# Performance work log

Hardware: AMD Instinct MI355X
Metric: run time of the kernel (lower is better)

## Reference

```python
import jax, jax.numpy as jnp
import numpy as np

IMG = 512
STRIDES = (8, 16, 32, 64, 128)
AREAS = np.array([(IMG // s) ** 2 for s in STRIDES])  # [4096,1024,256,64,16]
A_TOTAL = int(AREAS.sum())  # 5456
LEVELS = 5
TOP_K = 3
MAX_OBJ = 32
NUM_CLASSES = 80
BATCH = 16


def _detections():
    # [LEVELS, A_TOTAL] one-hot level membership per anchor (tf.pad of ones)
    det = np.zeros((LEVELS, A_TOTAL), np.float32)
    off = 0
    for i, a in enumerate(AREAS):
        det[i, off:off + a] = 1.0
        off += a
    return jnp.asarray(det)


def focal_loss(y_true, y_pred, alpha=0.25, gamma=2.0):
    # y_pred are sigmoid probabilities; sum over classes -> [B, A]
    p = jnp.clip(y_pred, 1e-7, 1.0 - 1e-7)
    ce = -(y_true * jnp.log(p) + (1.0 - y_true) * jnp.log(1.0 - p))
    alpha_t = y_true * alpha + (1.0 - y_true) * (1.0 - alpha)
    pt = y_true * (1.0 - p) + (1.0 - y_true) * p
    return jnp.sum(alpha_t * pt ** gamma * ce, axis=-1)


def giou_loss(y_true, y_pred):
    # ltrb distance encoding (all >= 0) -> per-anchor GIoU loss [B, A]
    tl, tt, tr, tb = (y_true[..., i] for i in range(4))
    pl, pt_, pr, pb = (y_pred[..., i] for i in range(4))
    area_t = (tl + tr) * (tt + tb)
    area_p = (pl + pr) * (pt_ + pb)
    inter = (jnp.minimum(tl, pl) + jnp.minimum(tr, pr)) * (jnp.minimum(tt, pt_) + jnp.minimum(tb, pb))
    union = area_t + area_p - inter
    iou = inter / jnp.maximum(union, 1e-7)
    enc = (jnp.maximum(tl, pl) + jnp.maximum(tr, pr)) * (jnp.maximum(tt, pt_) + jnp.maximum(tb, pb))
    giou = iou - (enc - union) / jnp.maximum(enc, 1e-7)
    return 1.0 - giou


def dwlm(total_loss, ind, bbox_cnt):
    # total_loss [B,A], ind [B,A] int, bbox_cnt [B] int
    det = _detections()                                   # [L, A]
    obj_ids = jnp.arange(MAX_OBJ)                         # [O]
    valid = obj_ids[None, :] < bbox_cnt[:, None]          # [B, O]
    obj_mask = (ind[:, None, :] == obj_ids[None, :, None]).astype(total_loss.dtype)  # [B,O,A]
    det_mask = obj_mask[:, :, None, :] * det[None, None]  # [B,O,L,A]
    obj_l_sum = jnp.einsum('ba,bola->bol', total_loss, det_mask)
    cnt = jnp.sum(det_mask, axis=-1)                      # [B,O,L]
    mean = obj_l_sum / jnp.maximum(1.0, cnt)
    lmax = jnp.max(mean, axis=-1, keepdims=True) + 1e-5
    mean = jnp.where(mean == 0.0, lmax, mean)
    lmin = jnp.min(mean, axis=-1, keepdims=True)
    target = 1.0 - (mean - lmin) / (lmax - lmin)          # [B,O,L]
    kth = jax.lax.top_k(target, TOP_K)[0][..., -1:]
    target = jnp.where(target >= kth, target, 0.0)
    target = jnp.where(valid[..., None], target, 0.0)     # drop padded objects
    return jnp.einsum('bol,bola->ba', target, det_mask)   # scatter-sum back to anchors


def setup_inputs() -> dict:
    key = jax.random.key(0)
    k = jax.random.split(key, 6)
    return {
        'cls_pred': jax.random.uniform(k[0], (BATCH, A_TOTAL, NUM_CLASSES), jnp.float32),
        'loc_pred': jax.random.uniform(k[1], (BATCH, A_TOTAL, 4), jnp.float32),
        'cls_tar': jax.random.uniform(k[2], (BATCH, A_TOTAL, NUM_CLASSES + 2), jnp.float32),
        'loc_tar': jax.random.uniform(k[3], (BATCH, A_TOTAL, 4), jnp.float32),
        'ind_tar': jax.random.randint(k[4], (BATCH, A_TOTAL, 1), 0, MAX_OBJ, jnp.int32),
        'bboxes_cnt': jax.random.randint(k[5], (BATCH, 1), 0, MAX_OBJ, jnp.int32),
    }


def reference(cls_pred, loc_pred, cls_tar, loc_tar, ind_tar, bboxes_cnt):
    cls_loss = focal_loss(cls_tar[..., :-2], cls_pred)
    loc_loss = giou_loss(loc_tar, loc_pred)
    dwlm_out = dwlm(cls_loss + loc_loss, ind_tar[..., 0], bboxes_cnt[..., 0])
    pos_mask = cls_tar[..., -1]
    dwlm_out_masked = jnp.where(pos_mask > 0.0, dwlm_out, 1.0)
    return dwlm_out_masked[..., None], pos_mask
```

## Files before the change

kernel.cpp:

```cpp
#include <hip/hip_runtime.h>

constexpr int A_TOTAL = 5456;
constexpr int BATCH = 16;
constexpr int NUM_CLASSES = 80;
constexpr int NUM_CH = NUM_CLASSES + 2;
constexpr int MAX_OBJ = 32;
constexpr int LEVELS = 5;
constexpr int BINS = MAX_OBJ * LEVELS;
constexpr int BLK_L = 1024;
constexpr int NSLOT = 16;
constexpr int APB = A_TOTAL / NSLOT;
constexpr int PASS = BLK_L / 4;
constexpr int BLK_G = 256;
constexpr int NBLK_G = (A_TOTAL + BLK_G - 1) / BLK_G;

__device__ __forceinline__ int lev_of(int a) {
    return (a < 4096) ? 0 : (a < 5120) ? 1 : (a < 5376) ? 2 : (a < 5440) ? 3 : 4;
}

__global__ void __launch_bounds__(BLK_L)
loss_accum_kernel(const float* __restrict__ cls_pred,
                  const float* __restrict__ loc_pred,
                  const float* __restrict__ cls_tar,
                  const float* __restrict__ loc_tar,
                  const int*   __restrict__ ind_tar,
                  float* __restrict__ p_sum,
                  float* __restrict__ p_cnt,
                  float* __restrict__ out) {
    __shared__ float s_sum[BINS];
    __shared__ float s_cnt[BINS];
    const int t = threadIdx.x;
    if (t < BINS) { s_sum[t] = 0.f; s_cnt[t] = 0.f; }
    __syncthreads();

    const int b = blockIdx.y;
    const int j = blockIdx.x;
    const int q = t & 3;
    const int r = t >> 2;

    #pragma unroll
    for (int base = 0; base < APB; base += PASS) {
        const int al = base + r;
        const bool valid = al < APB;

        float4 p4[5];
        float2 ta[5], tb[5];
        float4 T, P;
        float  pos = 0.f;
        size_t row = 0;
        int a = 0;

        if (valid) {
            a = j * APB + al;
            row = (size_t)b * A_TOTAL + a;
            const float4* pred4 = (const float4*)cls_pred + row * 20 + q;
            const float2* tar2  = (const float2*)cls_tar  + row * 41 + 2 * q;
            #pragma unroll
            for (int jj = 0; jj < 5; ++jj) {
                p4[jj] = pred4[4 * jj];
                ta[jj] = tar2[8 * jj];
                tb[jj] = tar2[8 * jj + 1];
            }
            T   = ((const float4*)(loc_tar  + row * 4))[0];
            P   = ((const float4*)(loc_pred + row * 4))[0];
            pos = cls_tar[row * NUM_CH + (NUM_CH - 1)];
        }

        float fl = 0.f;
        if (valid) {
            #pragma unroll
            for (int jj = 0; jj < 5; ++jj) {
                float ps[4] = {p4[jj].x, p4[jj].y, p4[jj].z, p4[jj].w};
                float ts[4] = {ta[jj].x, ta[jj].y, tb[jj].x, tb[jj].y};
                #pragma unroll
                for (int k = 0; k < 4; ++k) {
                    float p  = fminf(fmaxf(ps[k], 1e-7f), 1.0f - 1e-7f);
                    float tt = ts[k];
                    float ce = -(tt * __logf(p) + (1.f - tt) * __logf(1.f - p));
                    float alpha_t = tt * 0.25f + (1.f - tt) * 0.75f;
                    float pt = tt * (1.f - p) + (1.f - tt) * p;
                    fl += alpha_t * pt * pt * ce;
                }
            }
        }
        fl += __shfl_xor(fl, 1);
        fl += __shfl_xor(fl, 2);

        if (valid && q == 0) {
            out[(size_t)BATCH * A_TOTAL + row] = pos;

            float area_t = (T.x + T.z) * (T.y + T.w);
            float area_p = (P.x + P.z) * (P.y + P.w);
            float inter  = (fminf(T.x, P.x) + fminf(T.z, P.z)) * (fminf(T.y, P.y) + fminf(T.w, P.w));
            float uni    = area_t + area_p - inter;
            float iou    = inter / fmaxf(uni, 1e-7f);
            float enc    = (fmaxf(T.x, P.x) + fmaxf(T.z, P.z)) * (fmaxf(T.y, P.y) + fmaxf(T.w, P.w));
            float giou   = iou - (enc - uni) / fmaxf(enc, 1e-7f);
            float loss   = fl + (1.f - giou);

            int bin = ind_tar[row] * LEVELS + lev_of(a);
            atomicAdd(&s_sum[bin], loss);
            atomicAdd(&s_cnt[bin], 1.0f);
        }
    }
    __syncthreads();
    if (t < BINS) {
        const size_t slot = ((size_t)b * NSLOT + j) * BINS + t;
        p_sum[slot] = s_sum[t];
        p_cnt[slot] = s_cnt[t];
    }
}

__global__ void __launch_bounds__(BLK_G)
gather_kernel(const float* __restrict__ p_sum,
              const float* __restrict__ p_cnt,
              const int*   __restrict__ ind_tar,
              const int*   __restrict__ bbox_cnt,
              float* __restrict__ out) {
    __shared__ float s_mean[BINS];
    __shared__ float s_tgt[BINS];
    const int t = threadIdx.x;
    const int b = blockIdx.y;

    if (t < BINS) {
        float s = 0.f, c = 0.f;
        const size_t base = (size_t)b * NSLOT * BINS + t;
        #pragma unroll
        for (int k = 0; k < NSLOT; ++k) {
            s += p_sum[base + (size_t)k * BINS];
            c += p_cnt[base + (size_t)k * BINS];
        }
        s_mean[t] = s / fmaxf(1.0f, c);
    }
    __syncthreads();

    if (t < MAX_OBJ) {
        float mean[LEVELS];
        float mx = -1e30f;
        #pragma unroll
        for (int l = 0; l < LEVELS; ++l) {
            mean[l] = s_mean[t * LEVELS + l];
            mx = fmaxf(mx, mean[l]);
        }
        float lmax = mx + 1e-5f;
        float mn = 1e30f;
        #pragma unroll
        for (int l = 0; l < LEVELS; ++l) {
            if (mean[l] == 0.0f) mean[l] = lmax;
            mn = fminf(mn, mean[l]);
        }
        float denom = lmax - mn;
        float tgt[LEVELS];
        float m1 = -1e30f, m2 = -1e30f, m3 = -1e30f;
        #pragma unroll
        for (int l = 0; l < LEVELS; ++l) {
            float v = 1.0f - (mean[l] - mn) / denom;
            tgt[l] = v;
            if (v > m1)      { m3 = m2; m2 = m1; m1 = v; }
            else if (v > m2) { m3 = m2; m2 = v; }
            else if (v > m3) { m3 = v; }
        }
        const bool valid = t < bbox_cnt[b];
        #pragma unroll
        for (int l = 0; l < LEVELS; ++l) {
            float v = tgt[l];
            v = (v >= m3) ? v : 0.0f;
            s_tgt[t * LEVELS + l] = valid ? v : 0.0f;
        }
    }
    __syncthreads();

    const int a = blockIdx.x * BLK_G + t;
    if (a >= A_TOTAL) return;
    const size_t row = (size_t)b * A_TOTAL + a;
    float pos = out[(size_t)BATCH * A_TOTAL + row];
    int o = ind_tar[row];
    out[row] = (pos > 0.0f) ? s_tgt[o * LEVELS + lev_of(a)] : 1.0f;
}

extern "C" void kernel_launch(void* const* d_in, const int* in_sizes, int n_in,
                              void* d_out, int out_size, void* d_ws, size_t ws_size,
                              hipStream_t stream) {
    const float* cls_pred = (const float*)d_in[0];
    const float* loc_pred = (const float*)d_in[1];
    const float* cls_tar  = (const float*)d_in[2];
    const float* loc_tar  = (const float*)d_in[3];
    const int*   ind_tar  = (const int*)d_in[4];
    const int*   bbox_cnt = (const int*)d_in[5];
    float* out = (float*)d_out;

    float* p_sum = (float*)d_ws;
    float* p_cnt = p_sum + (size_t)BATCH * NSLOT * BINS;

    loss_accum_kernel<<<dim3(NSLOT, BATCH), dim3(BLK_L), 0, stream>>>(
        cls_pred, loc_pred, cls_tar, loc_tar, ind_tar, p_sum, p_cnt, out);
    gather_kernel<<<dim3(NBLK_G, BATCH), dim3(BLK_G), 0, stream>>>(
        p_sum, p_cnt, ind_tar, bbox_cnt, out);
}
```

Before: 20.59 us.

## Split each anchor across eight lanes, double slot count, use log2 focal math

Each anchor's 80 class values are now spread over eight lanes of ten values each instead of four lanes of twenty, and the per-batch anchors are split into 32 chunks of 171 instead of 16 chunks of 341. This doubles the grid and shortens each thread's dependent work. The focal loss is rewritten with log2 and simplified algebra, and the ln2 scaling is applied once per anchor. The gather kernel now reduces twice as many partial slots, and each lane's loads are 8-byte rather than 16-byte.

```diff
diff --git a/kernel.cpp b/kernel.cpp
--- a/kernel.cpp
+++ b/kernel.cpp
@@ -2,23 +2,44 @@
 
 constexpr int A_TOTAL = 5456;
 constexpr int BATCH = 16;
-constexpr int NUM_CLASSES = 80;
-constexpr int NUM_CH = NUM_CLASSES + 2;
+constexpr int NUM_CH = 82;
 constexpr int MAX_OBJ = 32;
 constexpr int LEVELS = 5;
 constexpr int BINS = MAX_OBJ * LEVELS;
 constexpr int BLK_L = 1024;
-constexpr int NSLOT = 16;
-constexpr int APB = A_TOTAL / NSLOT;
-constexpr int PASS = BLK_L / 4;
+constexpr int NSLOT = 32;
+constexpr int CH = 171;
+constexpr int PASS = BLK_L / 8;
 constexpr int BLK_G = 256;
 constexpr int NBLK_G = (A_TOTAL + BLK_G - 1) / BLK_G;
+constexpr float LN2 = 0.69314718056f;
 
 __device__ __forceinline__ int lev_of(int a) {
     return (a < 4096) ? 0 : (a < 5120) ? 1 : (a < 5376) ? 2 : (a < 5440) ? 3 : 4;
 }
 
-__global__ void __launch_bounds__(BLK_L)
+__device__ __forceinline__ float focal10(const float2* pv, const float2* tv) {
+    float fl = 0.f;
+    #pragma unroll
+    for (int jj = 0; jj < 5; ++jj) {
+        float ps[2] = {pv[jj].x, pv[jj].y};
+        float ts[2] = {tv[jj].x, tv[jj].y};
+        #pragma unroll
+        for (int k = 0; k < 2; ++k) {
+            float p  = fminf(fmaxf(ps[k], 1e-7f), 1.0f - 1e-7f);
+            float tt = ts[k];
+            float lp = __log2f(p);
+            float lq = __log2f(1.0f - p);
+            float ce2 = tt * (lp - lq) + lq;
+            float alpha_t = 0.75f - 0.5f * tt;
+            float pt = tt * (1.0f - 2.0f * p) + p;
+            fl += alpha_t * pt * pt * ce2;
+        }
+    }
+    return fl;
+}
+
+__global__ void __launch_bounds__(BLK_L, 8)
 loss_accum_kernel(const float* __restrict__ cls_pred,
                   const float* __restrict__ loc_pred,
                   const float* __restrict__ cls_tar,
@@ -35,60 +56,48 @@
 
     const int b = blockIdx.y;
     const int j = blockIdx.x;
-    const int q = t & 3;
-    const int r = t >> 2;
+    const int h = t & 7;
+    const int rr = t >> 3;
+    const int lim = min(CH, A_TOTAL - j * CH);
+
+    const char* predb = (const char*)cls_pred;
+    const char* tarb  = (const char*)cls_tar;
 
     #pragma unroll
-    for (int base = 0; base < APB; base += PASS) {
-        const int al = base + r;
-        const bool valid = al < APB;
-
-        float4 p4[5];
-        float2 ta[5], tb[5];
+    for (int base = 0; base < CH; base += PASS) {
+        const int al = base + rr;
+        const bool valid = al < lim;
+
+        float2 pv[5], tv[5];
         float4 T, P;
         float  pos = 0.f;
         size_t row = 0;
         int a = 0;
 
         if (valid) {
-            a = j * APB + al;
+            a = j * CH + al;
             row = (size_t)b * A_TOTAL + a;
-            const float4* pred4 = (const float4*)cls_pred + row * 20 + q;
-            const float2* tar2  = (const float2*)cls_tar  + row * 41 + 2 * q;
+            const char* pb = predb + row * 320 + h * 40;
+            const char* tb = tarb  + row * 328 + h * 40;
             #pragma unroll
             for (int jj = 0; jj < 5; ++jj) {
-                p4[jj] = pred4[4 * jj];
-                ta[jj] = tar2[8 * jj];
-                tb[jj] = tar2[8 * jj + 1];
+                pv[jj] = *(const float2*)(pb + 8 * jj);
+                tv[jj] = *(const float2*)(tb + 8 * jj);
             }
-            T   = ((const float4*)(loc_tar  + row * 4))[0];
-            P   = ((const float4*)(loc_pred + row * 4))[0];
-            pos = cls_tar[row * NUM_CH + (NUM_CH - 1)];
-        }
-
-        float fl = 0.f;
-        if (valid) {
-            #pragma unroll
-            for (int jj = 0; jj < 5; ++jj) {
-                float ps[4] = {p4[jj].x, p4[jj].y, p4[jj].z, p4[jj].w};
-                float ts[4] = {ta[jj].x, ta[jj].y, tb[jj].x, tb[jj].y};
-                #pragma unroll
-                for (int k = 0; k < 4; ++k) {
-                    float p  = fminf(fmaxf(ps[k], 1e-7f), 1.0f - 1e-7f);
-                    float tt = ts[k];
-                    float ce = -(tt * __logf(p) + (1.f - tt) * __logf(1.f - p));
-                    float alpha_t = tt * 0.25f + (1.f - tt) * 0.75f;
-                    float pt = tt * (1.f - p) + (1.f - tt) * p;
-                    fl += alpha_t * pt * pt * ce;
-                }
+            if (h == 0) {
+                T   = ((const float4*)(loc_tar  + row * 4))[0];
+                P   = ((const float4*)(loc_pred + row * 4))[0];
+                pos = cls_tar[row * NUM_CH + (NUM_CH - 1)];
             }
         }
+
+        float fl = valid ? focal10(pv, tv) : 0.f;
         fl += __shfl_xor(fl, 1);
         fl += __shfl_xor(fl, 2);
-
-        if (valid && q == 0) {
+        fl += __shfl_xor(fl, 4);
+
+        if (valid && h == 0) {
             out[(size_t)BATCH * A_TOTAL + row] = pos;
-
             float area_t = (T.x + T.z) * (T.y + T.w);
             float area_p = (P.x + P.z) * (P.y + P.w);
             float inter  = (fminf(T.x, P.x) + fminf(T.z, P.z)) * (fminf(T.y, P.y) + fminf(T.w, P.w));
@@ -96,13 +105,13 @@
             float iou    = inter / fmaxf(uni, 1e-7f);
             float enc    = (fmaxf(T.x, P.x) + fmaxf(T.z, P.z)) * (fmaxf(T.y, P.y) + fmaxf(T.w, P.w));
             float giou   = iou - (enc - uni) / fmaxf(enc, 1e-7f);
-            float loss   = fl + (1.f - giou);
-
+            float loss   = (1.f - giou) - LN2 * fl;
             int bin = ind_tar[row] * LEVELS + lev_of(a);
             atomicAdd(&s_sum[bin], loss);
             atomicAdd(&s_cnt[bin], 1.0f);
         }
     }
+
     __syncthreads();
     if (t < BINS) {
         const size_t slot = ((size_t)b * NSLOT + j) * BINS + t;
@@ -125,7 +134,7 @@
     if (t < BINS) {
         float s = 0.f, c = 0.f;
         const size_t base = (size_t)b * NSLOT * BINS + t;
-        #pragma unroll
+        #pragma unroll 8
         for (int k = 0; k < NSLOT; ++k) {
             s += p_sum[base + (size_t)k * BINS];
             c += p_cnt[base + (size_t)k * BINS];
```

Result: faster. 20.06 us (-2.6%).
